# Optimization experiments

Hardware: AMD Instinct MI355X
Metric: run time of the kernel (lower is better)

Reference implementation:

```python
import jax, jax.numpy as jnp
import numpy as np

N_NODES = 100000
N_EDGES = 1600000


def gcn_conv(x, W, b, src, dst, n):
    # PyG GCNConv: x @ W, add self-loops, symmetric deg^{-1/2} normalization,
    # sum-aggregate messages from src into dst, then add bias.
    h = x @ W  # [N, out]
    loops = jnp.arange(n, dtype=src.dtype)
    s = jnp.concatenate([src, loops])
    d = jnp.concatenate([dst, loops])
    deg = jax.ops.segment_sum(jnp.ones_like(d, dtype=h.dtype), d, num_segments=n)
    dinv = 1.0 / jnp.sqrt(deg)  # deg >= 1 thanks to self-loops
    norm = dinv[s] * dinv[d]  # [E + N]
    msg = h[s] * norm[:, None]
    out = jax.ops.segment_sum(msg, d, num_segments=n)
    return out + b


def setup_inputs() -> dict:
    key = jax.random.key(0)
    k1, k2, k3, k4 = jax.random.split(key, 4)
    x = jax.random.normal(k1, (N_NODES, 64), dtype=jnp.float32)
    edge_index = jax.random.randint(k2, (2, N_EDGES), 0, N_NODES, dtype=jnp.int64)
    W1 = jax.random.normal(k3, (64, 32), dtype=jnp.float32) * (1.0 / np.sqrt(64))
    b1 = jnp.zeros((32,), dtype=jnp.float32)
    W2 = jax.random.normal(k4, (32, 16), dtype=jnp.float32) * (1.0 / np.sqrt(32))
    b2 = jnp.zeros((16,), dtype=jnp.float32)
    return {"x": x, "edge_index": edge_index, "W1": W1, "b1": b1, "W2": W2, "b2": b2}


def reference(x, edge_index, W1, b1, W2, b2):
    n = x.shape[0]
    src, dst = edge_index[0], edge_index[1]
    h = gcn_conv(x, W1, b1, src, dst, n)
    h = jax.nn.relu(h)
    h = gcn_conv(h, W2, b2, src, dst, n)
    return jax.nn.log_softmax(h, axis=1)
```

## Files before the change

### kernel.cpp

```cpp
#include <hip/hip_runtime.h>
#include <hip/hip_bf16.h>


#define FEAT_IN 64
#define FEAT_H  32
#define FEAT_O  16
#define MAXNB   512
#define PART_G  256
#define MAXSNB  128

__device__ __forceinline__ float2 upk_bf2(unsigned w) {
    return make_float2(__uint_as_float(w << 16), __uint_as_float(w & 0xFFFF0000u));
}

__global__ void k_hist(const int* __restrict__ dst, int e,
                       int* __restrict__ hist, int G, int NBk) {
    __shared__ int lh[MAXNB];
    int t = threadIdx.x, g = blockIdx.x;
    for (int i = t; i < NBk; i += 256) lh[i] = 0;
    __syncthreads();
    int chunk = (e + G - 1) / G;
    int beg = g * chunk, end = min(e, beg + chunk);
    for (int i = beg + t; i < end; i += 256) atomicAdd(&lh[dst[i] >> 8], 1);
    __syncthreads();
    for (int i = t; i < NBk; i += 256) hist[(size_t)i * G + g] = lh[i];
}

__global__ void k_scan1(const int* __restrict__ in, int* __restrict__ out,
                        int* __restrict__ bsum, int len) {
    __shared__ int s[256];
    int t = threadIdx.x;
    int base = blockIdx.x * 1024 + t * 4;
    int a0 = (base + 0) < len ? in[base + 0] : 0;
    int a1 = (base + 1) < len ? in[base + 1] : 0;
    int a2 = (base + 2) < len ? in[base + 2] : 0;
    int a3 = (base + 3) < len ? in[base + 3] : 0;
    int tsum = a0 + a1 + a2 + a3;
    s[t] = tsum;
    __syncthreads();
    for (int off = 1; off < 256; off <<= 1) {
        int x = (t >= off) ? s[t - off] : 0;
        __syncthreads();
        s[t] += x;
        __syncthreads();
    }
    int ex = s[t] - tsum;
    if (base + 0 < len) out[base + 0] = ex;
    if (base + 1 < len) out[base + 1] = ex + a0;
    if (base + 2 < len) out[base + 2] = ex + a0 + a1;
    if (base + 3 < len) out[base + 3] = ex + a0 + a1 + a2;
    if (t == 255) bsum[blockIdx.x] = s[255];
}

__device__ __forceinline__ void scan_bsum(const int* __restrict__ bsum, int snb,
                                          int* __restrict__ sps, int t) {
    if (t < snb) sps[t] = bsum[t];
    __syncthreads();
    if (t == 0) {
        int acc = 0;
        for (int i = 0; i < snb; ++i) { int v = sps[i]; sps[i] = acc; acc += v; }
    }
    __syncthreads();
}

__global__ void k_partition(const int* __restrict__ src, const int* __restrict__ dst, int e,
                            const int* __restrict__ base, const int* __restrict__ bsum,
                            int snb, int* __restrict__ part, int G, int NBk) {
    __shared__ int cur[MAXNB];
    __shared__ int sps[MAXSNB];
    int t = threadIdx.x, g = blockIdx.x;
    scan_bsum(bsum, snb, sps, t);
    for (int i = t; i < NBk; i += 256) {
        size_t idx = (size_t)i * G + g;
        cur[i] = base[idx] + sps[idx >> 10];
    }
    __syncthreads();
    int chunk = (e + G - 1) / G;
    int beg = g * chunk, end = min(e, beg + chunk);
    for (int i = beg + t; i < end; i += 256) {
        int s_ = src[i], d_ = dst[i];
        int pos = atomicAdd(&cur[d_ >> 8], 1);
        part[pos] = s_ | ((d_ & 255) << 24);
    }
}

__global__ void k_bucket_csr(const int* __restrict__ part, const int* __restrict__ base,
                             const int* __restrict__ bsum, int snb, int e, int G, int NBk,
                             int n, int* __restrict__ row_start, int* __restrict__ col,
                             float* __restrict__ dinv) {
    __shared__ int cnt[256], spre[256], cur[256], ssc[256];
    __shared__ int sps[MAXSNB];
    int t = threadIdx.x, b = blockIdx.x;
    scan_bsum(bsum, snb, sps, t);
    size_t ib = (size_t)b * G;
    size_t ie = (size_t)(b + 1) * G;
    int beg = base[ib] + sps[ib >> 10];
    int end = (b == NBk - 1) ? e : (base[ie] + sps[ie >> 10]);
    cnt[t] = 0; cur[t] = 0;
    __syncthreads();
    for (int j = beg + t; j < end; j += 256) atomicAdd(&cnt[((unsigned)part[j]) >> 24], 1);
    __syncthreads();
    int v = cnt[t];
    ssc[t] = v;
    __syncthreads();
    for (int off = 1; off < 256; off <<= 1) {
        int x = (t >= off) ? ssc[t - off] : 0;
        __syncthreads();
        ssc[t] += x;
        __syncthreads();
    }
    spre[t] = ssc[t] - v;
    int node = b * 256 + t;
    if (node < n) {
        row_start[node] = beg + spre[t];
        dinv[node] = rsqrtf((float)v + 1.0f);
    }
    if (b == NBk - 1 && t == 0) row_start[n] = e;
    __syncthreads();
    for (int j = beg + t; j < end; j += 256) {
        int r = part[j];
        int dl = ((unsigned)r) >> 24;
        int off = atomicAdd(&cur[dl], 1);
        col[beg + spre[dl] + off] = r & 0x00FFFFFF;
    }
}

__global__ void k_gemm1(const float* __restrict__ x, const float* __restrict__ W1,
                        const float* __restrict__ dinv,
                        __hip_bfloat162* __restrict__ h1s2, int n) {
    __shared__ float sW[FEAT_IN * FEAT_H];
    __shared__ float sx[16][FEAT_IN + 1];
    int t = threadIdx.x;
    for (int i = t; i < FEAT_IN * FEAT_H; i += 256) sW[i] = W1[i];
#pragma unroll
    for (int tile = 0; tile < 2; ++tile) {
        int nodeBase = blockIdx.x * 32 + tile * 16;
        __syncthreads();
        {
            int xn = t >> 4, c = t & 15;
            int node = nodeBase + xn;
            if (node < n) {
                float4 v = ((const float4*)x)[(size_t)node * 16 + c];
                sx[xn][c * 4 + 0] = v.x; sx[xn][c * 4 + 1] = v.y;
                sx[xn][c * 4 + 2] = v.z; sx[xn][c * 4 + 3] = v.w;
            }
        }
        __syncthreads();
        int nl = t >> 4, g = t & 15;
        int node = nodeBase + nl;
        if (node < n) {
            float a0 = 0.0f, a1 = 0.0f;
#pragma unroll
            for (int k = 0; k < FEAT_IN; ++k) {
                float s = sx[nl][k];
                a0 += s * sW[k * FEAT_H + 2 * g];
                a1 += s * sW[k * FEAT_H + 2 * g + 1];
            }
            float dv = dinv[node];
            __hip_bfloat162 o;
            o.x = __float2bfloat16(a0 * dv);
            o.y = __float2bfloat16(a1 * dv);
            h1s2[(size_t)node * 16 + g] = o;
        }
    }
}

__global__ void k_gather1_gemm2(const int* __restrict__ row_start, const int* __restrict__ col,
                                const uint4* __restrict__ h1q, const float* __restrict__ W2,
                                const float* __restrict__ b1,
                                const float* __restrict__ dinv,
                                __hip_bfloat162* __restrict__ h2s2, int n) {
    __shared__ float sW[FEAT_H * FEAT_O];
    __shared__ float sb1[FEAT_H];
    __shared__ float sz[64][FEAT_H + 1];
    int t = threadIdx.x;
    for (int i = t; i < FEAT_H * FEAT_O; i += 256) sW[i] = W2[i];
    if (t < FEAT_H) sb1[t] = b1[t];
    __syncthreads();

    int g = t >> 2, l = t & 3;
    int d = blockIdx.x * 64 + g;
    if (d < n) {
        float a[8];
        {
            uint4 u = h1q[(size_t)d * 4 + l];
            float2 p;
            p = upk_bf2(u.x); a[0] = p.x; a[1] = p.y;
            p = upk_bf2(u.y); a[2] = p.x; a[3] = p.y;
            p = upk_bf2(u.z); a[4] = p.x; a[5] = p.y;
            p = upk_bf2(u.w); a[6] = p.x; a[7] = p.y;
        }
        int beg = row_start[d], end = row_start[d + 1];
        int j = beg;
        for (; j + 4 <= end; j += 4) {
            int c0 = col[j + 0], c1 = col[j + 1], c2 = col[j + 2], c3 = col[j + 3];
            uint4 u0 = h1q[(size_t)c0 * 4 + l];
            uint4 u1 = h1q[(size_t)c1 * 4 + l];
            uint4 u2 = h1q[(size_t)c2 * 4 + l];
            uint4 u3 = h1q[(size_t)c3 * 4 + l];
            float2 p;
            p = upk_bf2(u0.x); a[0] += p.x; a[1] += p.y;
            p = upk_bf2(u0.y); a[2] += p.x; a[3] += p.y;
            p = upk_bf2(u0.z); a[4] += p.x; a[5] += p.y;
            p = upk_bf2(u0.w); a[6] += p.x; a[7] += p.y;
            p = upk_bf2(u1.x); a[0] += p.x; a[1] += p.y;
            p = upk_bf2(u1.y); a[2] += p.x; a[3] += p.y;
            p = upk_bf2(u1.z); a[4] += p.x; a[5] += p.y;
            p = upk_bf2(u1.w); a[6] += p.x; a[7] += p.y;
            p = upk_bf2(u2.x); a[0] += p.x; a[1] += p.y;
            p = upk_bf2(u2.y); a[2] += p.x; a[3] += p.y;
            p = upk_bf2(u2.z); a[4] += p.x; a[5] += p.y;
            p = upk_bf2(u2.w); a[6] += p.x; a[7] += p.y;
            p = upk_bf2(u3.x); a[0] += p.x; a[1] += p.y;
            p = upk_bf2(u3.y); a[2] += p.x; a[3] += p.y;
            p = upk_bf2(u3.z); a[4] += p.x; a[5] += p.y;
            p = upk_bf2(u3.w); a[6] += p.x; a[7] += p.y;
        }
        for (; j < end; ++j) {
            uint4 u = h1q[(size_t)col[j] * 4 + l];
            float2 p;
            p = upk_bf2(u.x); a[0] += p.x; a[1] += p.y;
            p = upk_bf2(u.y); a[2] += p.x; a[3] += p.y;
            p = upk_bf2(u.z); a[4] += p.x; a[5] += p.y;
            p = upk_bf2(u.w); a[6] += p.x; a[7] += p.y;
        }
        float dv = dinv[d];
#pragma unroll
        for (int k = 0; k < 8; ++k)
            sz[g][l * 8 + k] = fmaxf(dv * a[k] + sb1[l * 8 + k], 0.0f);
    }
    __syncthreads();
#pragma unroll
    for (int it = 0; it < 2; ++it) {
        int nl = (t >> 3) + it * 32;
        int m = t & 7;
        int node = blockIdx.x * 64 + nl;
        if (node < n) {
            float a0 = 0.0f, a1 = 0.0f;
#pragma unroll
            for (int f = 0; f < FEAT_H; ++f) {
                float z = sz[nl][f];
                a0 += z * sW[f * FEAT_O + 2 * m];
                a1 += z * sW[f * FEAT_O + 2 * m + 1];
            }
            float dv = dinv[node];
            __hip_bfloat162 o;
            o.x = __float2bfloat16(a0 * dv);
            o.y = __float2bfloat16(a1 * dv);
            h2s2[(size_t)node * 8 + m] = o;
        }
    }
}

__global__ void k_gather2_lsm(const int* __restrict__ row_start, const int* __restrict__ col,
                              const uint4* __restrict__ h2q, const float* __restrict__ b2,
                              const float* __restrict__ dinv,
                              float4* __restrict__ out4, int n) {
    __shared__ float sb2[FEAT_O];
    int t = threadIdx.x;
    if (t < FEAT_O) sb2[t] = b2[t];
    __syncthreads();
    int g = t >> 1, h = t & 1;
    int d = blockIdx.x * 128 + g;
    if (d >= n) return;
    float a[8];
    {
        uint4 u = h2q[(size_t)d * 2 + h];
        float2 p;
        p = upk_bf2(u.x); a[0] = p.x; a[1] = p.y;
        p = upk_bf2(u.y); a[2] = p.x; a[3] = p.y;
        p = upk_bf2(u.z); a[4] = p.x; a[5] = p.y;
        p = upk_bf2(u.w); a[6] = p.x; a[7] = p.y;
    }
    int beg = row_start[d], end = row_start[d + 1];
    int j = beg;
    for (; j + 4 <= end; j += 4) {
        int c0 = col[j + 0], c1 = col[j + 1], c2 = col[j + 2], c3 = col[j + 3];
        uint4 u0 = h2q[(size_t)c0 * 2 + h];
        uint4 u1 = h2q[(size_t)c1 * 2 + h];
        uint4 u2 = h2q[(size_t)c2 * 2 + h];
        uint4 u3 = h2q[(size_t)c3 * 2 + h];
        float2 p;
        p = upk_bf2(u0.x); a[0] += p.x; a[1] += p.y;
        p = upk_bf2(u0.y); a[2] += p.x; a[3] += p.y;
        p = upk_bf2(u0.z); a[4] += p.x; a[5] += p.y;
        p = upk_bf2(u0.w); a[6] += p.x; a[7] += p.y;
        p = upk_bf2(u1.x); a[0] += p.x; a[1] += p.y;
        p = upk_bf2(u1.y); a[2] += p.x; a[3] += p.y;
        p = upk_bf2(u1.z); a[4] += p.x; a[5] += p.y;
        p = upk_bf2(u1.w); a[6] += p.x; a[7] += p.y;
        p = upk_bf2(u2.x); a[0] += p.x; a[1] += p.y;
        p = upk_bf2(u2.y); a[2] += p.x; a[3] += p.y;
        p = upk_bf2(u2.z); a[4] += p.x; a[5] += p.y;
        p = upk_bf2(u2.w); a[6] += p.x; a[7] += p.y;
        p = upk_bf2(u3.x); a[0] += p.x; a[1] += p.y;
        p = upk_bf2(u3.y); a[2] += p.x; a[3] += p.y;
        p = upk_bf2(u3.z); a[4] += p.x; a[5] += p.y;
        p = upk_bf2(u3.w); a[6] += p.x; a[7] += p.y;
    }
    for (; j < end; ++j) {
        uint4 u = h2q[(size_t)col[j] * 2 + h];
        float2 p;
        p = upk_bf2(u.x); a[0] += p.x; a[1] += p.y;
        p = upk_bf2(u.y); a[2] += p.x; a[3] += p.y;
        p = upk_bf2(u.z); a[4] += p.x; a[5] += p.y;
        p = upk_bf2(u.w); a[6] += p.x; a[7] += p.y;
    }
    float dv = dinv[d];
    float v[8];
    float mx = -1e30f;
#pragma unroll
    for (int k = 0; k < 8; ++k) {
        v[k] = dv * a[k] + sb2[h * 8 + k];
        mx = fmaxf(mx, v[k]);
    }
    mx = fmaxf(mx, __shfl_xor(mx, 1));
    float ssum = 0.0f;
#pragma unroll
    for (int k = 0; k < 8; ++k) ssum += __expf(v[k] - mx);
    ssum += __shfl_xor(ssum, 1);
    float lg = mx + logf(ssum);
    float4 o0 = { v[0] - lg, v[1] - lg, v[2] - lg, v[3] - lg };
    float4 o1 = { v[4] - lg, v[5] - lg, v[6] - lg, v[7] - lg };
    out4[(size_t)d * 4 + h * 2 + 0] = o0;
    out4[(size_t)d * 4 + h * 2 + 1] = o1;
}

extern "C" void kernel_launch(void* const* d_in, const int* in_sizes, int n_in,
                              void* d_out, int out_size, void* d_ws, size_t ws_size,
                              hipStream_t stream) {
    const float* x  = (const float*)d_in[0];
    const int*   ei = (const int*)d_in[1];
    const float* W1 = (const float*)d_in[2];
    const float* b1 = (const float*)d_in[3];
    const float* W2 = (const float*)d_in[4];
    const float* b2 = (const float*)d_in[5];

    const int n = in_sizes[0] / FEAT_IN;
    const int e = in_sizes[1] / 2;
    const int* src = ei;
    const int* dst = ei + e;
    const int NBk = (n + 255) >> 8;
    const int G = PART_G;
    const int hlen = NBk * G;
    const int snb = (hlen + 1023) / 1024;

    int* part = (int*)d_ws;
    __hip_bfloat162* h1s2 = (__hip_bfloat162*)d_ws;
    int* col  = (int*)d_ws + e;
    __hip_bfloat162* h2s2 = (__hip_bfloat162*)(col + e);
    float* dinv = (float*)(h2s2 + 8 * (size_t)n);
    int* hist      = (int*)(dinv + n);
    int* base      = hist + hlen;
    int* bsum      = base + hlen;
    int* row_start = bsum + MAXSNB;

    k_hist<<<G, 256, 0, stream>>>(dst, e, hist, G, NBk);
    k_scan1<<<snb, 256, 0, stream>>>(hist, base, bsum, hlen);
    k_partition<<<G, 256, 0, stream>>>(src, dst, e, base, bsum, snb, part, G, NBk);
    k_bucket_csr<<<NBk, 256, 0, stream>>>(part, base, bsum, snb, e, G, NBk, n,
                                          row_start, col, dinv);

    k_gemm1<<<(n + 31) / 32, 256, 0, stream>>>(x, W1, dinv, h1s2, n);
    k_gather1_gemm2<<<(n + 63) / 64, 256, 0, stream>>>(row_start, col, (const uint4*)h1s2,
                                                       W2, b1, dinv, h2s2, n);
    k_gather2_lsm<<<(n + 127) / 128, 256, 0, stream>>>(row_start, col, (const uint4*)h2s2,
                                                       b2, dinv, (float4*)d_out, n);
}
```

Before: 185.2 us.

## Replace two-pass bucket partition CSR build with global-atomic degree count and fill

Swaps the bucketed histogram, partition and per-bucket CSR construction for a direct approach: global atomic degree counting, a prefix scan over per-node degrees, and an atomic-cursor scatter of source indices into the column array. This drops the intermediate partition buffer and one full pass over the edges. In exchange it relies on 1.6M global atomics per pass instead of shared-memory atomics, and the order of neighbours within each row becomes nondeterministic, which can change float summation order.

```diff
diff --git a/kernel.cpp b/kernel.cpp
--- a/kernel.cpp
+++ b/kernel.cpp
@@ -5,25 +5,24 @@
 #define FEAT_IN 64
 #define FEAT_H  32
 #define FEAT_O  16
-#define MAXNB   512
-#define PART_G  256
 #define MAXSNB  128
 
 __device__ __forceinline__ float2 upk_bf2(unsigned w) {
     return make_float2(__uint_as_float(w << 16), __uint_as_float(w & 0xFFFF0000u));
 }
 
-__global__ void k_hist(const int* __restrict__ dst, int e,
-                       int* __restrict__ hist, int G, int NBk) {
-    __shared__ int lh[MAXNB];
-    int t = threadIdx.x, g = blockIdx.x;
-    for (int i = t; i < NBk; i += 256) lh[i] = 0;
-    __syncthreads();
-    int chunk = (e + G - 1) / G;
-    int beg = g * chunk, end = min(e, beg + chunk);
-    for (int i = beg + t; i < end; i += 256) atomicAdd(&lh[dst[i] >> 8], 1);
-    __syncthreads();
-    for (int i = t; i < NBk; i += 256) hist[(size_t)i * G + g] = lh[i];
+__global__ void k_deg(const int4* __restrict__ dst4, int e4, int rem, const int* __restrict__ dst_tail,
+                      int* __restrict__ deg) {
+    int i = blockIdx.x * blockDim.x + threadIdx.x;
+    int stride = gridDim.x * blockDim.x;
+    for (int j = i; j < e4; j += stride) {
+        int4 d = dst4[j];
+        atomicAdd(&deg[d.x], 1);
+        atomicAdd(&deg[d.y], 1);
+        atomicAdd(&deg[d.z], 1);
+        atomicAdd(&deg[d.w], 1);
+    }
+    if (blockIdx.x == 0 && threadIdx.x < rem) atomicAdd(&deg[dst_tail[threadIdx.x]], 1);
 }
 
 __global__ void k_scan1(const int* __restrict__ in, int* __restrict__ out,
@@ -63,66 +62,39 @@
     __syncthreads();
 }
 
-__global__ void k_partition(const int* __restrict__ src, const int* __restrict__ dst, int e,
-                            const int* __restrict__ base, const int* __restrict__ bsum,
-                            int snb, int* __restrict__ part, int G, int NBk) {
-    __shared__ int cur[MAXNB];
+__global__ void k_fix(const int* __restrict__ ebase, const int* __restrict__ bsum, int snb,
+                      const int* __restrict__ deg, int n, int e,
+                      int* __restrict__ row_start, int* __restrict__ cursor,
+                      float* __restrict__ dinv) {
     __shared__ int sps[MAXSNB];
-    int t = threadIdx.x, g = blockIdx.x;
+    int t = threadIdx.x;
     scan_bsum(bsum, snb, sps, t);
-    for (int i = t; i < NBk; i += 256) {
-        size_t idx = (size_t)i * G + g;
-        cur[i] = base[idx] + sps[idx >> 10];
-    }
-    __syncthreads();
-    int chunk = (e + G - 1) / G;
-    int beg = g * chunk, end = min(e, beg + chunk);
-    for (int i = beg + t; i < end; i += 256) {
-        int s_ = src[i], d_ = dst[i];
-        int pos = atomicAdd(&cur[d_ >> 8], 1);
-        part[pos] = s_ | ((d_ & 255) << 24);
-    }
-}
-
-__global__ void k_bucket_csr(const int* __restrict__ part, const int* __restrict__ base,
-                             const int* __restrict__ bsum, int snb, int e, int G, int NBk,
-                             int n, int* __restrict__ row_start, int* __restrict__ col,
-                             float* __restrict__ dinv) {
-    __shared__ int cnt[256], spre[256], cur[256], ssc[256];
-    __shared__ int sps[MAXSNB];
-    int t = threadIdx.x, b = blockIdx.x;
-    scan_bsum(bsum, snb, sps, t);
-    size_t ib = (size_t)b * G;
-    size_t ie = (size_t)(b + 1) * G;
-    int beg = base[ib] + sps[ib >> 10];
-    int end = (b == NBk - 1) ? e : (base[ie] + sps[ie >> 10]);
-    cnt[t] = 0; cur[t] = 0;
-    __syncthreads();
-    for (int j = beg + t; j < end; j += 256) atomicAdd(&cnt[((unsigned)part[j]) >> 24], 1);
-    __syncthreads();
-    int v = cnt[t];
-    ssc[t] = v;
-    __syncthreads();
-    for (int off = 1; off < 256; off <<= 1) {
-        int x = (t >= off) ? ssc[t - off] : 0;
-        __syncthreads();
-        ssc[t] += x;
-        __syncthreads();
-    }
-    spre[t] = ssc[t] - v;
-    int node = b * 256 + t;
-    if (node < n) {
-        row_start[node] = beg + spre[t];
-        dinv[node] = rsqrtf((float)v + 1.0f);
-    }
-    if (b == NBk - 1 && t == 0) row_start[n] = e;
-    __syncthreads();
-    for (int j = beg + t; j < end; j += 256) {
-        int r = part[j];
-        int dl = ((unsigned)r) >> 24;
-        int off = atomicAdd(&cur[dl], 1);
-        col[beg + spre[dl] + off] = r & 0x00FFFFFF;
-    }
+    int i = blockIdx.x * 256 + t;
+    if (i < n) {
+        int r = ebase[i] + sps[i >> 10];
+        row_start[i] = r;
+        cursor[i] = r;
+        dinv[i] = rsqrtf((float)deg[i] + 1.0f);
+    }
+    if (blockIdx.x == 0 && t == 0) row_start[n] = e;
+}
+
+__global__ void k_fill(const int4* __restrict__ src4, const int4* __restrict__ dst4,
+                       int e4, int rem, const int* __restrict__ src_tail,
+                       const int* __restrict__ dst_tail,
+                       int* __restrict__ cursor, int* __restrict__ col) {
+    int i = blockIdx.x * blockDim.x + threadIdx.x;
+    int stride = gridDim.x * blockDim.x;
+    for (int j = i; j < e4; j += stride) {
+        int4 s = src4[j];
+        int4 d = dst4[j];
+        col[atomicAdd(&cursor[d.x], 1)] = s.x;
+        col[atomicAdd(&cursor[d.y], 1)] = s.y;
+        col[atomicAdd(&cursor[d.z], 1)] = s.z;
+        col[atomicAdd(&cursor[d.w], 1)] = s.w;
+    }
+    if (blockIdx.x == 0 && threadIdx.x < rem)
+        col[atomicAdd(&cursor[dst_tail[threadIdx.x]], 1)] = src_tail[threadIdx.x];
 }
 
 __global__ void k_gemm1(const float* __restrict__ x, const float* __restrict__ W1,
@@ -340,26 +312,26 @@
     const int e = in_sizes[1] / 2;
     const int* src = ei;
     const int* dst = ei + e;
-    const int NBk = (n + 255) >> 8;
-    const int G = PART_G;
-    const int hlen = NBk * G;
-    const int snb = (hlen + 1023) / 1024;
-
-    int* part = (int*)d_ws;
-    __hip_bfloat162* h1s2 = (__hip_bfloat162*)d_ws;
-    int* col  = (int*)d_ws + e;
-    __hip_bfloat162* h2s2 = (__hip_bfloat162*)(col + e);
+    const int snb = (n + 1023) / 1024;
+    const int e4 = e >> 2, rem = e & 3;
+
+    int* col = (int*)d_ws;
+    __hip_bfloat162* h1s2 = (__hip_bfloat162*)(col + e);
+    __hip_bfloat162* h2s2 = h1s2 + 16 * (size_t)n;
     float* dinv = (float*)(h2s2 + 8 * (size_t)n);
-    int* hist      = (int*)(dinv + n);
-    int* base      = hist + hlen;
-    int* bsum      = base + hlen;
+    int* deg       = (int*)(dinv + n);
+    int* ebase     = deg + n;
+    int* bsum      = ebase + n;
     int* row_start = bsum + MAXSNB;
-
-    k_hist<<<G, 256, 0, stream>>>(dst, e, hist, G, NBk);
-    k_scan1<<<snb, 256, 0, stream>>>(hist, base, bsum, hlen);
-    k_partition<<<G, 256, 0, stream>>>(src, dst, e, base, bsum, snb, part, G, NBk);
-    k_bucket_csr<<<NBk, 256, 0, stream>>>(part, base, bsum, snb, e, G, NBk, n,
-                                          row_start, col, dinv);
+    int* cursor    = row_start + n + 1;
+
+    hipMemsetAsync(deg, 0, (size_t)n * sizeof(int), stream);
+    k_deg<<<1024, 256, 0, stream>>>((const int4*)dst, e4, rem, dst + e4 * 4, deg);
+    k_scan1<<<snb, 256, 0, stream>>>(deg, ebase, bsum, n);
+    k_fix<<<(n + 255) / 256, 256, 0, stream>>>(ebase, bsum, snb, deg, n, e,
+                                               row_start, cursor, dinv);
+    k_fill<<<1024, 256, 0, stream>>>((const int4*)src, (const int4*)dst, e4, rem,
+                                     src + e4 * 4, dst + e4 * 4, cursor, col);
 
     k_gemm1<<<(n + 31) / 32, 256, 0, stream>>>(x, W1, dinv, h1s2, n);
     k_gather1_gemm2<<<(n + 63) / 64, 256, 0, stream>>>(row_start, col, (const uint4*)h1s2,
```

Measured after the change: 331.5 us. 1.79x slower.

## Replace per-node CSR build with bucketed shared-memory atomic aggregation

Applied to the files above, without the earlier changes.

Drops the second sorting pass that produced a per-node CSR (row_start/col). Edges stay only partitioned into 256-node destination buckets, and each aggregation kernel runs one 1024-thread block per bucket that scatter-adds gathered source features into a shared-memory accumulator with LDS atomics. This removes the global col writes and the intra-bucket counting sort, but brings LDS atomic contention, only 391 blocks, and per-element 2-byte gathers instead of 16-byte vector loads.

```diff
diff --git a/kernel.cpp b/kernel.cpp
--- a/kernel.cpp
+++ b/kernel.cpp
@@ -63,6 +63,15 @@
     __syncthreads();
 }
 
+__global__ void k_fixb(const int* __restrict__ base, const int* __restrict__ bsum,
+                       int snb, int G, int NBk, int e, int* __restrict__ bucket_start) {
+    __shared__ int sps[MAXSNB];
+    int t = threadIdx.x;
+    scan_bsum(bsum, snb, sps, t);
+    for (int i = t; i <= NBk; i += 256)
+        bucket_start[i] = (i == NBk) ? e : (base[(size_t)i * G] + sps[(i * G) >> 10]);
+}
+
 __global__ void k_partition(const int* __restrict__ src, const int* __restrict__ dst, int e,
                             const int* __restrict__ base, const int* __restrict__ bsum,
                             int snb, int* __restrict__ part, int G, int NBk) {
@@ -84,45 +93,17 @@
     }
 }
 
-__global__ void k_bucket_csr(const int* __restrict__ part, const int* __restrict__ base,
-                             const int* __restrict__ bsum, int snb, int e, int G, int NBk,
-                             int n, int* __restrict__ row_start, int* __restrict__ col,
-                             float* __restrict__ dinv) {
-    __shared__ int cnt[256], spre[256], cur[256], ssc[256];
-    __shared__ int sps[MAXSNB];
+__global__ void k_bdeg(const int* __restrict__ part, const int* __restrict__ bucket_start,
+                       int n, float* __restrict__ dinv) {
+    __shared__ int cnt[256];
     int t = threadIdx.x, b = blockIdx.x;
-    scan_bsum(bsum, snb, sps, t);
-    size_t ib = (size_t)b * G;
-    size_t ie = (size_t)(b + 1) * G;
-    int beg = base[ib] + sps[ib >> 10];
-    int end = (b == NBk - 1) ? e : (base[ie] + sps[ie >> 10]);
-    cnt[t] = 0; cur[t] = 0;
-    __syncthreads();
-    for (int j = beg + t; j < end; j += 256) atomicAdd(&cnt[((unsigned)part[j]) >> 24], 1);
-    __syncthreads();
-    int v = cnt[t];
-    ssc[t] = v;
-    __syncthreads();
-    for (int off = 1; off < 256; off <<= 1) {
-        int x = (t >= off) ? ssc[t - off] : 0;
-        __syncthreads();
-        ssc[t] += x;
-        __syncthreads();
-    }
-    spre[t] = ssc[t] - v;
-    int node = b * 256 + t;
-    if (node < n) {
-        row_start[node] = beg + spre[t];
-        dinv[node] = rsqrtf((float)v + 1.0f);
-    }
-    if (b == NBk - 1 && t == 0) row_start[n] = e;
-    __syncthreads();
-    for (int j = beg + t; j < end; j += 256) {
-        int r = part[j];
-        int dl = ((unsigned)r) >> 24;
-        int off = atomicAdd(&cur[dl], 1);
-        col[beg + spre[dl] + off] = r & 0x00FFFFFF;
-    }
+    cnt[t] = 0;
+    int bs = bucket_start[b], be = bucket_start[b + 1];
+    __syncthreads();
+    for (int j = bs + t; j < be; j += 256) atomicAdd(&cnt[((unsigned)part[j]) >> 24], 1);
+    __syncthreads();
+    int d = b * 256 + t;
+    if (d < n) dinv[d] = rsqrtf((float)cnt[t] + 1.0f);
 }
 
 __global__ void k_gemm1(const float* __restrict__ x, const float* __restrict__ W1,
@@ -165,81 +146,58 @@
     }
 }
 
-__global__ void k_gather1_gemm2(const int* __restrict__ row_start, const int* __restrict__ col,
-                                const uint4* __restrict__ h1q, const float* __restrict__ W2,
-                                const float* __restrict__ b1,
-                                const float* __restrict__ dinv,
-                                __hip_bfloat162* __restrict__ h2s2, int n) {
+__global__ void __launch_bounds__(1024)
+k_agg1(const int* __restrict__ part, const int* __restrict__ bucket_start,
+       const uint4* __restrict__ h1q, const unsigned short* __restrict__ h1u,
+       const float* __restrict__ W2, const float* __restrict__ b1,
+       const float* __restrict__ dinv, __hip_bfloat162* __restrict__ h2s2, int n) {
+    __shared__ float acc[256 * 33];
     __shared__ float sW[FEAT_H * FEAT_O];
     __shared__ float sb1[FEAT_H];
-    __shared__ float sz[64][FEAT_H + 1];
-    int t = threadIdx.x;
-    for (int i = t; i < FEAT_H * FEAT_O; i += 256) sW[i] = W2[i];
+    int t = threadIdx.x, b = blockIdx.x;
+    for (int i = t; i < FEAT_H * FEAT_O; i += 1024) sW[i] = W2[i];
     if (t < FEAT_H) sb1[t] = b1[t];
-    __syncthreads();
-
-    int g = t >> 2, l = t & 3;
-    int d = blockIdx.x * 64 + g;
-    if (d < n) {
-        float a[8];
-        {
-            uint4 u = h1q[(size_t)d * 4 + l];
+    for (int i = t; i < 256 * 33; i += 1024) acc[i] = 0.0f;
+    int bs = bucket_start[b], be = bucket_start[b + 1];
+    __syncthreads();
+    int grp = t >> 5, q = t & 31;
+    for (int j = bs + grp; j < be; j += 32) {
+        int r = part[j];
+        int s = r & 0x00FFFFFF;
+        int dl = ((unsigned)r) >> 24;
+        float v = __uint_as_float((unsigned)h1u[(size_t)s * 32 + q] << 16);
+        atomicAdd(&acc[dl * 33 + q], v);
+    }
+    __syncthreads();
+    {
+        int nl = t >> 2, lf = t & 3;
+        int d = b * 256 + nl;
+        if (d < n) {
+            uint4 u = h1q[(size_t)d * 4 + lf];
+            float dv = dinv[d];
+            float sf[8];
             float2 p;
-            p = upk_bf2(u.x); a[0] = p.x; a[1] = p.y;
-            p = upk_bf2(u.y); a[2] = p.x; a[3] = p.y;
-            p = upk_bf2(u.z); a[4] = p.x; a[5] = p.y;
-            p = upk_bf2(u.w); a[6] = p.x; a[7] = p.y;
+            p = upk_bf2(u.x); sf[0] = p.x; sf[1] = p.y;
+            p = upk_bf2(u.y); sf[2] = p.x; sf[3] = p.y;
+            p = upk_bf2(u.z); sf[4] = p.x; sf[5] = p.y;
+            p = upk_bf2(u.w); sf[6] = p.x; sf[7] = p.y;
+            int base = nl * 33 + lf * 8;
+#pragma unroll
+            for (int k = 0; k < 8; ++k)
+                acc[base + k] = fmaxf(dv * (acc[base + k] + sf[k]) + sb1[lf * 8 + k], 0.0f);
         }
-        int beg = row_start[d], end = row_start[d + 1];
-        int j = beg;
-        for (; j + 4 <= end; j += 4) {
-            int c0 = col[j + 0], c1 = col[j + 1], c2 = col[j + 2], c3 = col[j + 3];
-            uint4 u0 = h1q[(size_t)c0 * 4 + l];
-            uint4 u1 = h1q[(size_t)c1 * 4 + l];
-            uint4 u2 = h1q[(size_t)c2 * 4 + l];
-            uint4 u3 = h1q[(size_t)c3 * 4 + l];
-            float2 p;
-            p = upk_bf2(u0.x); a[0] += p.x; a[1] += p.y;
-            p = upk_bf2(u0.y); a[2] += p.x; a[3] += p.y;
-            p = upk_bf2(u0.z); a[4] += p.x; a[5] += p.y;
-            p = upk_bf2(u0.w); a[6] += p.x; a[7] += p.y;
-            p = upk_bf2(u1.x); a[0] += p.x; a[1] += p.y;
-            p = upk_bf2(u1.y); a[2] += p.x; a[3] += p.y;
-            p = upk_bf2(u1.z); a[4] += p.x; a[5] += p.y;
-            p = upk_bf2(u1.w); a[6] += p.x; a[7] += p.y;
-            p = upk_bf2(u2.x); a[0] += p.x; a[1] += p.y;
-            p = upk_bf2(u2.y); a[2] += p.x; a[3] += p.y;
-            p = upk_bf2(u2.z); a[4] += p.x; a[5] += p.y;
-            p = upk_bf2(u2.w); a[6] += p.x; a[7] += p.y;
-            p = upk_bf2(u3.x); a[0] += p.x; a[1] += p.y;
-            p = upk_bf2(u3.y); a[2] += p.x; a[3] += p.y;
-            p = upk_bf2(u3.z); a[4] += p.x; a[5] += p.y;
-            p = upk_bf2(u3.w); a[6] += p.x; a[7] += p.y;
-        }
-        for (; j < end; ++j) {
-            uint4 u = h1q[(size_t)col[j] * 4 + l];
-            float2 p;
-            p = upk_bf2(u.x); a[0] += p.x; a[1] += p.y;
-            p = upk_bf2(u.y); a[2] += p.x; a[3] += p.y;
-            p = upk_bf2(u.z); a[4] += p.x; a[5] += p.y;
-            p = upk_bf2(u.w); a[6] += p.x; a[7] += p.y;
-        }
-        float dv = dinv[d];
-#pragma unroll
-        for (int k = 0; k < 8; ++k)
-            sz[g][l * 8 + k] = fmaxf(dv * a[k] + sb1[l * 8 + k], 0.0f);
     }
     __syncthreads();
 #pragma unroll
     for (int it = 0; it < 2; ++it) {
-        int nl = (t >> 3) + it * 32;
+        int nl = (t >> 3) + it * 128;
         int m = t & 7;
-        int node = blockIdx.x * 64 + nl;
+        int node = b * 256 + nl;
         if (node < n) {
             float a0 = 0.0f, a1 = 0.0f;
 #pragma unroll
             for (int f = 0; f < FEAT_H; ++f) {
-                float z = sz[nl][f];
+                float z = acc[nl * 33 + f];
                 a0 += z * sW[f * FEAT_O + 2 * m];
                 a1 += z * sW[f * FEAT_O + 2 * m + 1];
             }
@@ -252,78 +210,53 @@
     }
 }
 
-__global__ void k_gather2_lsm(const int* __restrict__ row_start, const int* __restrict__ col,
-                              const uint4* __restrict__ h2q, const float* __restrict__ b2,
-                              const float* __restrict__ dinv,
-                              float4* __restrict__ out4, int n) {
+__global__ void __launch_bounds__(1024)
+k_agg2(const int* __restrict__ part, const int* __restrict__ bucket_start,
+       const uint2* __restrict__ h2q2, const unsigned short* __restrict__ h2u,
+       const float* __restrict__ b2, const float* __restrict__ dinv,
+       float4* __restrict__ out4, int n) {
+    __shared__ float acc[256 * 17];
     __shared__ float sb2[FEAT_O];
-    int t = threadIdx.x;
+    int t = threadIdx.x, b = blockIdx.x;
     if (t < FEAT_O) sb2[t] = b2[t];
-    __syncthreads();
-    int g = t >> 1, h = t & 1;
-    int d = blockIdx.x * 128 + g;
+    for (int i = t; i < 256 * 17; i += 1024) acc[i] = 0.0f;
+    int bs = bucket_start[b], be = bucket_start[b + 1];
+    __syncthreads();
+    int grp = t >> 4, q = t & 15;
+    for (int j = bs + grp; j < be; j += 64) {
+        int r = part[j];
+        int s = r & 0x00FFFFFF;
+        int dl = ((unsigned)r) >> 24;
+        float v = __uint_as_float((unsigned)h2u[(size_t)s * 16 + q] << 16);
+        atomicAdd(&acc[dl * 17 + q], v);
+    }
+    __syncthreads();
+    int nl = t >> 2, lf = t & 3;
+    int d = b * 256 + nl;
     if (d >= n) return;
-    float a[8];
-    {
-        uint4 u = h2q[(size_t)d * 2 + h];
-        float2 p;
-        p = upk_bf2(u.x); a[0] = p.x; a[1] = p.y;
-        p = upk_bf2(u.y); a[2] = p.x; a[3] = p.y;
-        p = upk_bf2(u.z); a[4] = p.x; a[5] = p.y;
-        p = upk_bf2(u.w); a[6] = p.x; a[7] = p.y;
-    }
-    int beg = row_start[d], end = row_start[d + 1];
-    int j = beg;
-    for (; j + 4 <= end; j += 4) {
-        int c0 = col[j + 0], c1 = col[j + 1], c2 = col[j + 2], c3 = col[j + 3];
-        uint4 u0 = h2q[(size_t)c0 * 2 + h];
-        uint4 u1 = h2q[(size_t)c1 * 2 + h];
-        uint4 u2 = h2q[(size_t)c2 * 2 + h];
-        uint4 u3 = h2q[(size_t)c3 * 2 + h];
-        float2 p;
-        p = upk_bf2(u0.x); a[0] += p.x; a[1] += p.y;
-        p = upk_bf2(u0.y); a[2] += p.x; a[3] += p.y;
-        p = upk_bf2(u0.z); a[4] += p.x; a[5] += p.y;
-        p = upk_bf2(u0.w); a[6] += p.x; a[7] += p.y;
-        p = upk_bf2(u1.x); a[0] += p.x; a[1] += p.y;
-        p = upk_bf2(u1.y); a[2] += p.x; a[3] += p.y;
-        p = upk_bf2(u1.z); a[4] += p.x; a[5] += p.y;
-        p = upk_bf2(u1.w); a[6] += p.x; a[7] += p.y;
-        p = upk_bf2(u2.x); a[0] += p.x; a[1] += p.y;
-        p = upk_bf2(u2.y); a[2] += p.x; a[3] += p.y;
-        p = upk_bf2(u2.z); a[4] += p.x; a[5] += p.y;
-        p = upk_bf2(u2.w); a[6] += p.x; a[7] += p.y;
-        p = upk_bf2(u3.x); a[0] += p.x; a[1] += p.y;
-        p = upk_bf2(u3.y); a[2] += p.x; a[3] += p.y;
-        p = upk_bf2(u3.z); a[4] += p.x; a[5] += p.y;
-        p = upk_bf2(u3.w); a[6] += p.x; a[7] += p.y;
-    }
-    for (; j < end; ++j) {
-        uint4 u = h2q[(size_t)col[j] * 2 + h];
-        float2 p;
-        p = upk_bf2(u.x); a[0] += p.x; a[1] += p.y;
-        p = upk_bf2(u.y); a[2] += p.x; a[3] += p.y;
-        p = upk_bf2(u.z); a[4] += p.x; a[5] += p.y;
-        p = upk_bf2(u.w); a[6] += p.x; a[7] += p.y;
-    }
+    uint2 u = h2q2[(size_t)d * 4 + lf];
     float dv = dinv[d];
-    float v[8];
+    float vv[4];
+    float2 p;
+    p = upk_bf2(u.x); vv[0] = p.x; vv[1] = p.y;
+    p = upk_bf2(u.y); vv[2] = p.x; vv[3] = p.y;
+    int base = nl * 17 + lf * 4;
     float mx = -1e30f;
 #pragma unroll
-    for (int k = 0; k < 8; ++k) {
-        v[k] = dv * a[k] + sb2[h * 8 + k];
-        mx = fmaxf(mx, v[k]);
+    for (int k = 0; k < 4; ++k) {
+        vv[k] = dv * (acc[base + k] + vv[k]) + sb2[lf * 4 + k];
+        mx = fmaxf(mx, vv[k]);
     }
     mx = fmaxf(mx, __shfl_xor(mx, 1));
+    mx = fmaxf(mx, __shfl_xor(mx, 2));
     float ssum = 0.0f;
 #pragma unroll
-    for (int k = 0; k < 8; ++k) ssum += __expf(v[k] - mx);
+    for (int k = 0; k < 4; ++k) ssum += __expf(vv[k] - mx);
     ssum += __shfl_xor(ssum, 1);
+    ssum += __shfl_xor(ssum, 2);
     float lg = mx + logf(ssum);
-    float4 o0 = { v[0] - lg, v[1] - lg, v[2] - lg, v[3] - lg };
-    float4 o1 = { v[4] - lg, v[5] - lg, v[6] - lg, v[7] - lg };
-    out4[(size_t)d * 4 + h * 2 + 0] = o0;
-    out4[(size_t)d * 4 + h * 2 + 1] = o1;
+    float4 o = { vv[0] - lg, vv[1] - lg, vv[2] - lg, vv[3] - lg };
+    out4[(size_t)d * 4 + lf] = o;
 }
 
 extern "C" void kernel_launch(void* const* d_in, const int* in_sizes, int n_in,
@@ -346,24 +279,24 @@
     const int snb = (hlen + 1023) / 1024;
 
     int* part = (int*)d_ws;
-    __hip_bfloat162* h1s2 = (__hip_bfloat162*)d_ws;
-    int* col  = (int*)d_ws + e;
-    __hip_bfloat162* h2s2 = (__hip_bfloat162*)(col + e);
+    __hip_bfloat162* h1s2 = (__hip_bfloat162*)(part + e);
+    __hip_bfloat162* h2s2 = h1s2 + 16 * (size_t)n;
     float* dinv = (float*)(h2s2 + 8 * (size_t)n);
-    int* hist      = (int*)(dinv + n);
-    int* base      = hist + hlen;
-    int* bsum      = base + hlen;
-    int* row_start = bsum + MAXSNB;
+    int* hist         = (int*)(dinv + n);
+    int* base         = hist + hlen;
+    int* bsum         = base + hlen;
+    int* bucket_start = bsum + MAXSNB;
 
     k_hist<<<G, 256, 0, stream>>>(dst, e, hist, G, NBk);
     k_scan1<<<snb, 256, 0, stream>>>(hist, base, bsum, hlen);
+    k_fixb<<<1, 256, 0, stream>>>(base, bsum, snb, G, NBk, e, bucket_start);
     k_partition<<<G, 256, 0, stream>>>(src, dst, e, base, bsum, snb, part, G, NBk);
-    k_bucket_csr<<<NBk, 256, 0, stream>>>(part, base, bsum, snb, e, G, NBk, n,
-                                          row_start, col, dinv);
+    k_bdeg<<<NBk, 256, 0, stream>>>(part, bucket_start, n, dinv);
 
     k_gemm1<<<(n + 31) / 32, 256, 0, stream>>>(x, W1, dinv, h1s2, n);
-    k_gather1_gemm2<<<(n + 63) / 64, 256, 0, stream>>>(row_start, col, (const uint4*)h1s2,
-                                                       W2, b1, dinv, h2s2, n);
-    k_gather2_lsm<<<(n + 127) / 128, 256, 0, stream>>>(row_start, col, (const uint4*)h2s2,
-                                                       b2, dinv, (float4*)d_out, n);
-}
+    k_agg1<<<NBk, 1024, 0, stream>>>(part, bucket_start, (const uint4*)h1s2,
+                                     (const unsigned short*)h1s2, W2, b1, dinv, h2s2, n);
+    k_agg2<<<NBk, 1024, 0, stream>>>(part, bucket_start, (const uint2*)h2s2,
+                                     (const unsigned short*)h2s2, b2, dinv,
+                                     (float4*)d_out, n);
+}
```

Result: slower. 662.5 us (+257.7%).
